# Performance work log

Measured on AMD Instinct MI355X. Metric: run time of the kernel, lower is better.

## Reference

```python
import jax, jax.numpy as jnp
import numpy as np

NEG_BIG = -9e15
LRELU_SLOPE = 0.2  # alpha

N = 8192
IN_F = 256
OUT_F = 128


def setup_inputs() -> dict:
    key = jax.random.key(0)
    k1, k2, k3, k4 = jax.random.split(key, 4)
    inputs = jax.random.normal(k1, (N, IN_F), dtype=jnp.float32)
    adj = jax.random.randint(k2, (N, N), 0, 2, dtype=jnp.int32)
    # xavier_uniform with gain=1.414
    gain = 1.414
    bW = gain * np.sqrt(6.0 / (IN_F + OUT_F))
    W = jax.random.uniform(k3, (IN_F, OUT_F), minval=-bW, maxval=bW, dtype=jnp.float32)
    ba = gain * np.sqrt(6.0 / (2 * OUT_F + 1))
    a = jax.random.uniform(k4, (2 * OUT_F, 1), minval=-ba, maxval=ba, dtype=jnp.float32)
    return {"inputs": inputs, "adj": adj, "W": W, "a": a}


def reference(inputs, adj, W, a):
    # h: [N, F']
    h = inputs @ W
    # a^T [h_i || h_j] = h_i . a[:F'] + h_j . a[F':]  -- avoids the O(N^2 * 2F') concat
    a1 = a[:OUT_F, 0]   # [F']
    a2 = a[OUT_F:, 0]   # [F']
    s1 = h @ a1         # [N]
    s2 = h @ a2         # [N]
    e = s1[:, None] + s2[None, :]                      # [N, N]
    e = jnp.where(e >= 0, e, LRELU_SLOPE * e)          # LeakyReLU(alpha)
    scores = jnp.where(adj > 0, e, jnp.float32(NEG_BIG))
    attention = jax.nn.softmax(scores, axis=1)         # row softmax; dropout p=0
    h_prime = attention @ h                            # [N, F']
    return jax.nn.elu(h_prime)                         # concat=True -> elu
```

## Files before the change

kernel.cpp:

```cpp
#include <hip/hip_runtime.h>
#include <hip/hip_bf16.h>

#define NN   8192
#define INF_ 256
#define OUTF 128
#define SLOPE 0.2f
#define NJC  4
#define JCHUNK (NN / NJC)
#define NT   (JCHUNK / 128)

typedef float f32x4  __attribute__((ext_vector_type(4)));
typedef float f32x16 __attribute__((ext_vector_type(16)));
typedef short bf16x8 __attribute__((ext_vector_type(8)));
typedef int   i32x4  __attribute__((ext_vector_type(4)));
typedef unsigned short u16;
typedef u16 u16x4 __attribute__((ext_vector_type(4)));

__device__ __forceinline__ u16 f2bf(float f) {
  return __builtin_bit_cast(u16, __float2bfloat16(f));
}


__global__ __launch_bounds__(256) void gat_k0(const int* __restrict__ adj,
                                              unsigned char* __restrict__ bm) {
  const int idx = blockIdx.x * 256 + threadIdx.x;
  const int r  = idx >> 10;
  const int jg = idx & 1023;
  const int* p = adj + (size_t)r * NN + jg * 8;
  i32x4 a0 = *(const i32x4*)p;
  i32x4 a1 = *(const i32x4*)(p + 4);
  unsigned b = 0;
#pragma unroll
  for (int e = 0; e < 4; e++) b |= (a0[e] > 0 ? 1u : 0u) << e;
#pragma unroll
  for (int e = 0; e < 4; e++) b |= (a1[e] > 0 ? 1u : 0u) << (e + 4);
  bm[(size_t)r * 1024 + jg] = (unsigned char)b;
}

__global__ __launch_bounds__(256) void gat_k1(
    const float* __restrict__ X, const float* __restrict__ W,
    const float* __restrict__ a, u16* __restrict__ hbF,
    float* __restrict__ s1, float* __restrict__ s2) {
  __shared__ float xs[32 * INF_];
  const int t = threadIdx.x;
  const int r0 = blockIdx.x * 32;
  {
    const f32x4* src = (const f32x4*)(X + (size_t)r0 * INF_);
    f32x4* dst = (f32x4*)xs;
    for (int i = t; i < 32 * INF_ / 4; i += 256) dst[i] = src[i];
  }
  __syncthreads();
  const int cg = t & 31;
  const int rg = t >> 5;
  float acc[4][4];
#pragma unroll
  for (int i = 0; i < 4; i++)
#pragma unroll
    for (int j = 0; j < 4; j++) acc[i][j] = 0.f;

  for (int k = 0; k < INF_; k += 4) {
    f32x4 xv[4];
#pragma unroll
    for (int i = 0; i < 4; i++) xv[i] = *(const f32x4*)&xs[(rg * 4 + i) * INF_ + k];
#pragma unroll
    for (int kk = 0; kk < 4; kk++) {
      f32x4 wv = *(const f32x4*)&W[(k + kk) * OUTF + cg * 4];
#pragma unroll
      for (int i = 0; i < 4; i++)
#pragma unroll
        for (int j = 0; j < 4; j++) acc[i][j] = fmaf(xv[i][kk], wv[j], acc[i][j]);
    }
  }

  f32x4 a1v = *(const f32x4*)&a[cg * 4];
  f32x4 a2v = *(const f32x4*)&a[OUTF + cg * 4];
  float p1[4], p2[4];
#pragma unroll
  for (int i = 0; i < 4; i++) {
    p1[i] = acc[i][0] * a1v[0] + acc[i][1] * a1v[1] + acc[i][2] * a1v[2] + acc[i][3] * a1v[3];
    p2[i] = acc[i][0] * a2v[0] + acc[i][1] * a2v[1] + acc[i][2] * a2v[2] + acc[i][3] * a2v[3];
  }
#pragma unroll
  for (int m = 1; m < 32; m <<= 1) {
#pragma unroll
    for (int i = 0; i < 4; i++) {
      p1[i] += __shfl_xor(p1[i], m);
      p2[i] += __shfl_xor(p2[i], m);
    }
  }
  if (cg == 0) {
#pragma unroll
    for (int i = 0; i < 4; i++) {
      s1[r0 + rg * 4 + i] = p1[i];
      s2[r0 + rg * 4 + i] = p2[i];
    }
  }

  const int R0 = r0 + rg * 4;
  const int jg = (R0 & 2047) >> 3;
  const int tt = jg & 15;
  const int pr = jg >> 4;
  const int wq = pr >> 1;
  const int gg = pr & 1;
  const int e0 = R0 & 7;
  const int n  = ((R0 >> 11) * 16 + tt) * 8 + wq;
#pragma unroll
  for (int j = 0; j < 4; j++) {
    const int C = cg * 4 + j;
    u16x4 pk;
#pragma unroll
    for (int i = 0; i < 4; i++) pk[i] = f2bf(acc[i][j]);
    size_t flat = ((size_t)(n * 4 + (C >> 5)) * 64 + (C & 31) + 32 * gg) * 8 + e0;
    *(u16x4*)(hbF + flat) = pk;
  }
}

__global__ __launch_bounds__(256) void gat_k2(const float* __restrict__ s2,
                                              float* __restrict__ s2m) {
  __shared__ float sm[4];
  const int t = threadIdx.x;
  float m = -1e30f;
  for (int i = t; i < NN; i += 256) m = fmaxf(m, s2[i]);
#pragma unroll
  for (int k = 1; k < 64; k <<= 1) m = fmaxf(m, __shfl_xor(m, k));
  if ((t & 63) == 0) sm[t >> 6] = m;
  __syncthreads();
  if (t == 0) *s2m = fmaxf(fmaxf(sm[0], sm[1]), fmaxf(sm[2], sm[3]));
}

__device__ __forceinline__ void st16(float* dst, const f32x16& A, int g) {
#pragma unroll
  for (int r = 0; r < 16; r++) {
    const int dr = (r & 3) + 8 * (r >> 2) + 4 * g;
    dst[dr * 128] = A[r];
  }
}
__device__ __forceinline__ void ad16(float* dst, const f32x16& A, int g) {
#pragma unroll
  for (int r = 0; r < 16; r++) {
    const int dr = (r & 3) + 8 * (r >> 2) + 4 * g;
    dst[dr * 128] += A[r];
  }
}

__global__ __launch_bounds__(512, 2) void gat_k3(
    const unsigned char* __restrict__ bm, const u16* __restrict__ hbF,
    const float* __restrict__ s1g, const float* __restrict__ s2g,
    const float* __restrict__ s2maxp, float* __restrict__ part,
    float* __restrict__ dpart) {
  __shared__ float lred[8192];
  __shared__ float dred[256];
  const int t = threadIdx.x;
  const int w = t >> 6;
  const int l = t & 63;
  const int rb = blockIdx.x & 255;
  const int jc = blockIdx.x >> 8;
  const int r0 = rb * 32;
  const int row = l & 31;
  const int g = l >> 5;

  const float s1r = s1g[r0 + row];
  const float s2m = *s2maxp;
  float Mi = s1r + s2m;
  Mi = fmaxf(Mi, SLOPE * Mi);
  const float ar = s1r - Mi;
  const float br = SLOPE * s1r - Mi;

  const int pr = 2 * w + g;
  const i32x4 bmv = *(const i32x4*)(bm + (size_t)(r0 + row) * 1024 +
                                    jc * 256 + pr * 16);

  f32x16 acc0 = 0.f, acc1 = 0.f, acc2 = 0.f, acc3 = 0.f;

  const float* sp = s2g + jc * JCHUNK + pr * 128;
  const bf16x8* bp = (const bf16x8*)hbF + ((size_t)(jc * 128 + w) * 4) * 64 + l;

  float dsum = 0.f;
#pragma unroll
  for (int q4 = 0; q4 < 4; q4++) {
    const unsigned word = (unsigned)bmv[q4];
#pragma unroll
    for (int ti = 0; ti < 4; ti++) {
      const int tt = q4 * 4 + ti;
      const unsigned b = (word >> (ti * 8)) & 0xffu;
      const bf16x8* bq = bp + (size_t)tt * 2048;
      bf16x8 b0 = bq[0], b1 = bq[64], b2 = bq[128], b3 = bq[192];
      f32x4 s0  = *(const f32x4*)(sp + 8 * tt);
      f32x4 s1v = *(const f32x4*)(sp + 8 * tt + 4);

      bf16x8 af;
#pragma unroll
      for (int e = 0; e < 8; e++) {
        const float sv = (e < 4) ? s0[e] : s1v[e - 4];
        const float y = fmaxf(ar + sv, fmaf(SLOPE, sv, br));
        float p = __expf(y);
        p = ((b >> e) & 1u) ? p : 0.f;
        dsum += p;
        af[e] = (short)f2bf(p);
      }
      acc0 = __builtin_amdgcn_mfma_f32_32x32x16_bf16(af, b0, acc0, 0, 0, 0);
      acc1 = __builtin_amdgcn_mfma_f32_32x32x16_bf16(af, b1, acc1, 0, 0, 0);
      acc2 = __builtin_amdgcn_mfma_f32_32x32x16_bf16(af, b2, acc2, 0, 0, 0);
      acc3 = __builtin_amdgcn_mfma_f32_32x32x16_bf16(af, b3, acc3, 0, 0, 0);
    }
  }

  dsum += __shfl_xor(dsum, 32);
  if (l < 32) dred[w * 32 + l] = dsum;

  const int colw = l & 31;
  if (w < 2) {
    st16(&lred[w * 4096 + 0 * 32 + colw], acc0, g);
    st16(&lred[w * 4096 + 1 * 32 + colw], acc1, g);
    st16(&lred[w * 4096 + 2 * 32 + colw], acc2, g);
    st16(&lred[w * 4096 + 3 * 32 + colw], acc3, g);
  }
  __syncthreads();
  if (t < 32) {
    float d = 0.f;
#pragma unroll
    for (int w8 = 0; w8 < 8; w8++) d += dred[w8 * 32 + t];
    dpart[jc * NN + r0 + t] = d;
  }
  if (w == 2 || w == 3) {
    ad16(&lred[(w - 2) * 4096 + 0 * 32 + colw], acc0, g);
    ad16(&lred[(w - 2) * 4096 + 1 * 32 + colw], acc1, g);
    ad16(&lred[(w - 2) * 4096 + 2 * 32 + colw], acc2, g);
    ad16(&lred[(w - 2) * 4096 + 3 * 32 + colw], acc3, g);
  }
  __syncthreads();
  if (w == 4 || w == 5) {
    ad16(&lred[(w - 4) * 4096 + 0 * 32 + colw], acc0, g);
    ad16(&lred[(w - 4) * 4096 + 1 * 32 + colw], acc1, g);
    ad16(&lred[(w - 4) * 4096 + 2 * 32 + colw], acc2, g);
    ad16(&lred[(w - 4) * 4096 + 3 * 32 + colw], acc3, g);
  }
  __syncthreads();
  if (w == 6 || w == 7) {
    ad16(&lred[(w - 6) * 4096 + 0 * 32 + colw], acc0, g);
    ad16(&lred[(w - 6) * 4096 + 1 * 32 + colw], acc1, g);
    ad16(&lred[(w - 6) * 4096 + 2 * 32 + colw], acc2, g);
    ad16(&lred[(w - 6) * 4096 + 3 * 32 + colw], acc3, g);
  }
  __syncthreads();

  const int flat = t * 8;
  f32x4 pa = *(f32x4*)&lred[flat];
  f32x4 pb = *(f32x4*)&lred[flat + 4];
  pa += *(f32x4*)&lred[4096 + flat];
  pb += *(f32x4*)&lred[4096 + flat + 4];
  float* pp = part + (size_t)jc * (NN * OUTF) + (size_t)r0 * OUTF + flat;
  *(f32x4*)pp = pa;
  *(f32x4*)(pp + 4) = pb;
}

__global__ __launch_bounds__(256) void gat_k4(
    const float* __restrict__ part, const float* __restrict__ dpart,
    float* __restrict__ out) {
  const int idx = blockIdx.x * 256 + threadIdx.x;
  const int e4 = idx * 4;
  const int i = e4 >> 7;
  f32x4 p = {0.f, 0.f, 0.f, 0.f};
  float d = 0.f;
#pragma unroll
  for (int jc = 0; jc < NJC; jc++) {
    p += *(const f32x4*)&part[(size_t)jc * (NN * OUTF) + e4];
    d += dpart[jc * NN + i];
  }
  d = fmaxf(d, 1e-30f);
  f32x4 r;
#pragma unroll
  for (int k = 0; k < 4; k++) {
    float v = p[k] / d;
    r[k] = (v > 0.f) ? v : expm1f(v);
  }
  *(f32x4*)&out[e4] = r;
}

extern "C" void kernel_launch(void* const* d_in, const int* in_sizes, int n_in,
                              void* d_out, int out_size, void* d_ws, size_t ws_size,
                              hipStream_t stream) {
  (void)in_sizes; (void)n_in; (void)out_size; (void)ws_size;
  const float* X  = (const float*)d_in[0];
  const int*  adj = (const int*)d_in[1];
  const float* W  = (const float*)d_in[2];
  const float* a  = (const float*)d_in[3];
  float* out = (float*)d_out;

  char* ws = (char*)d_ws;
  u16*   hbF   = (u16*)ws;
  float* s1    = (float*)(ws + (2u << 20));
  float* s2    = (float*)(ws + (2u << 20) + (32u << 10));
  float* s2m   = (float*)(ws + (2u << 20) + (64u << 10));
  float* dpart = (float*)(ws + (2u << 20) + (128u << 10));
  unsigned char* bm = (unsigned char*)(ws + (3u << 20));
  float* part  = (float*)(ws + (12u << 20));

  gat_k0<<<NN * 1024 / 256, 256, 0, stream>>>(adj, bm);
  gat_k1<<<NN / 32, 256, 0, stream>>>(X, W, a, hbF, s1, s2);
  gat_k2<<<1, 256, 0, stream>>>(s2, s2m);
  gat_k3<<<256 * NJC, 512, 0, stream>>>(bm, hbF, s1, s2, s2m, part, dpart);
  gat_k4<<<(NN * OUTF / 4) / 256, 256, 0, stream>>>(part, dpart, out);
}
```

Before: 120.0 us.

## Factor per-element exp into precomputed column exponentials and raise occupancy

The main loop computed exp(max(s1-M + s2, 0.2*s1-M + 0.2*s2)) for every (row, col) pair. It now computes max(A*exp(s2), B*exp(0.2*s2)), which removes the per-element transcendental from the hot loop. The column exponentials E1 and E2 are computed once in the s2-max kernel, which now runs with 1024 threads and vector loads. The loop also converts to bf16 with a cheap add-and-byte-permute instead of the library conversion, and raises the minimum-blocks hint to 4. Costs and risks: the hot loop now reads twice as many column values. exp(s2) can overflow or underflow where the fused exponent would not. The stricter occupancy hint may force the 64 accumulator registers to spill.

```diff
diff --git a/kernel.cpp b/kernel.cpp
--- a/kernel.cpp
+++ b/kernel.cpp
@@ -13,6 +13,7 @@
 typedef float f32x16 __attribute__((ext_vector_type(16)));
 typedef short bf16x8 __attribute__((ext_vector_type(8)));
 typedef int   i32x4  __attribute__((ext_vector_type(4)));
+typedef unsigned int u32;
 typedef unsigned short u16;
 typedef u16 u16x4 __attribute__((ext_vector_type(4)));
 
@@ -115,17 +116,35 @@
   }
 }
 
-__global__ __launch_bounds__(256) void gat_k2(const float* __restrict__ s2,
-                                              float* __restrict__ s2m) {
-  __shared__ float sm[4];
+__global__ __launch_bounds__(1024) void gat_k2(const float* __restrict__ s2,
+                                               float* __restrict__ s2m,
+                                               float* __restrict__ E1,
+                                               float* __restrict__ E2) {
+  __shared__ float sm[16];
   const int t = threadIdx.x;
   float m = -1e30f;
-  for (int i = t; i < NN; i += 256) m = fmaxf(m, s2[i]);
+  for (int i = t; i < NN / 4; i += 1024) {
+    f32x4 v = ((const f32x4*)s2)[i];
+    f32x4 e1, e2;
+#pragma unroll
+    for (int k = 0; k < 4; k++) {
+      m = fmaxf(m, v[k]);
+      e1[k] = __expf(v[k]);
+      e2[k] = __expf(SLOPE * v[k]);
+    }
+    ((f32x4*)E1)[i] = e1;
+    ((f32x4*)E2)[i] = e2;
+  }
 #pragma unroll
   for (int k = 1; k < 64; k <<= 1) m = fmaxf(m, __shfl_xor(m, k));
   if ((t & 63) == 0) sm[t >> 6] = m;
   __syncthreads();
-  if (t == 0) *s2m = fmaxf(fmaxf(sm[0], sm[1]), fmaxf(sm[2], sm[3]));
+  if (t == 0) {
+    float mm = sm[0];
+#pragma unroll
+    for (int k = 1; k < 16; k++) mm = fmaxf(mm, sm[k]);
+    *s2m = mm;
+  }
 }
 
 __device__ __forceinline__ void st16(float* dst, const f32x16& A, int g) {
@@ -143,11 +162,11 @@
   }
 }
 
-__global__ __launch_bounds__(512, 2) void gat_k3(
+__global__ __launch_bounds__(512, 4) void gat_k3(
     const unsigned char* __restrict__ bm, const u16* __restrict__ hbF,
-    const float* __restrict__ s1g, const float* __restrict__ s2g,
-    const float* __restrict__ s2maxp, float* __restrict__ part,
-    float* __restrict__ dpart) {
+    const float* __restrict__ s1g, const float* __restrict__ E1,
+    const float* __restrict__ E2, const float* __restrict__ s2maxp,
+    float* __restrict__ part, float* __restrict__ dpart) {
   __shared__ float lred[8192];
   __shared__ float dred[256];
   const int t = threadIdx.x;
@@ -163,8 +182,8 @@
   const float s2m = *s2maxp;
   float Mi = s1r + s2m;
   Mi = fmaxf(Mi, SLOPE * Mi);
-  const float ar = s1r - Mi;
-  const float br = SLOPE * s1r - Mi;
+  const float A = __expf(s1r - Mi);
+  const float B = __expf(SLOPE * s1r - Mi);
 
   const int pr = 2 * w + g;
   const i32x4 bmv = *(const i32x4*)(bm + (size_t)(r0 + row) * 1024 +
@@ -172,38 +191,50 @@
 
   f32x16 acc0 = 0.f, acc1 = 0.f, acc2 = 0.f, acc3 = 0.f;
 
-  const float* sp = s2g + jc * JCHUNK + pr * 128;
+  const float* e1p = E1 + jc * JCHUNK + pr * 128;
+  const float* e2p = E2 + jc * JCHUNK + pr * 128;
   const bf16x8* bp = (const bf16x8*)hbF + ((size_t)(jc * 128 + w) * 4) * 64 + l;
 
-  float dsum = 0.f;
+  float dsA = 0.f, dsB = 0.f;
 #pragma unroll
   for (int q4 = 0; q4 < 4; q4++) {
     const unsigned word = (unsigned)bmv[q4];
 #pragma unroll
     for (int ti = 0; ti < 4; ti++) {
       const int tt = q4 * 4 + ti;
-      const unsigned b = (word >> (ti * 8)) & 0xffu;
+      const unsigned b = word >> (ti * 8);
       const bf16x8* bq = bp + (size_t)tt * 2048;
       bf16x8 b0 = bq[0], b1 = bq[64], b2 = bq[128], b3 = bq[192];
-      f32x4 s0  = *(const f32x4*)(sp + 8 * tt);
-      f32x4 s1v = *(const f32x4*)(sp + 8 * tt + 4);
-
-      bf16x8 af;
-#pragma unroll
-      for (int e = 0; e < 8; e++) {
-        const float sv = (e < 4) ? s0[e] : s1v[e - 4];
-        const float y = fmaxf(ar + sv, fmaf(SLOPE, sv, br));
-        float p = __expf(y);
-        p = ((b >> e) & 1u) ? p : 0.f;
-        dsum += p;
-        af[e] = (short)f2bf(p);
+      f32x4 u0 = *(const f32x4*)(e1p + 8 * tt);
+      f32x4 u1 = *(const f32x4*)(e1p + 8 * tt + 4);
+      f32x4 v0 = *(const f32x4*)(e2p + 8 * tt);
+      f32x4 v1 = *(const f32x4*)(e2p + 8 * tt + 4);
+      const float uu[8] = {u0[0], u0[1], u0[2], u0[3], u1[0], u1[1], u1[2], u1[3]};
+      const float vv[8] = {v0[0], v0[1], v0[2], v0[3], v1[0], v1[1], v1[2], v1[3]};
+
+      u32 aw[4];
+#pragma unroll
+      for (int e = 0; e < 8; e += 2) {
+        float pa = fmaxf(A * uu[e],     B * vv[e]);
+        float pb = fmaxf(A * uu[e + 1], B * vv[e + 1]);
+        pa = (b & (1u << e))       ? pa : 0.f;
+        pb = (b & (1u << (e + 1))) ? pb : 0.f;
+        dsA += pa;
+        dsB += pb;
+        aw[e >> 1] = __builtin_amdgcn_perm(
+            __builtin_bit_cast(u32, pb) + 0x8000u,
+            __builtin_bit_cast(u32, pa) + 0x8000u, 0x07060302u);
       }
+      const bf16x8 af =
+          __builtin_bit_cast(bf16x8, (i32x4){(int)aw[0], (int)aw[1],
+                                             (int)aw[2], (int)aw[3]});
       acc0 = __builtin_amdgcn_mfma_f32_32x32x16_bf16(af, b0, acc0, 0, 0, 0);
       acc1 = __builtin_amdgcn_mfma_f32_32x32x16_bf16(af, b1, acc1, 0, 0, 0);
       acc2 = __builtin_amdgcn_mfma_f32_32x32x16_bf16(af, b2, acc2, 0, 0, 0);
       acc3 = __builtin_amdgcn_mfma_f32_32x32x16_bf16(af, b3, acc3, 0, 0, 0);
     }
   }
+  float dsum = dsA + dsB;
 
   dsum += __shfl_xor(dsum, 32);
   if (l < 32) dred[w * 32 + l] = dsum;
@@ -292,13 +323,15 @@
   float* s1    = (float*)(ws + (2u << 20));
   float* s2    = (float*)(ws + (2u << 20) + (32u << 10));
   float* s2m   = (float*)(ws + (2u << 20) + (64u << 10));
-  float* dpart = (float*)(ws + (2u << 20) + (128u << 10));
+  float* E1    = (float*)(ws + (2u << 20) + (128u << 10));
+  float* E2    = (float*)(ws + (2u << 20) + (160u << 10));
+  float* dpart = (float*)(ws + (2u << 20) + (192u << 10));
   unsigned char* bm = (unsigned char*)(ws + (3u << 20));
   float* part  = (float*)(ws + (12u << 20));
 
   gat_k0<<<NN * 1024 / 256, 256, 0, stream>>>(adj, bm);
   gat_k1<<<NN / 32, 256, 0, stream>>>(X, W, a, hbF, s1, s2);
-  gat_k2<<<1, 256, 0, stream>>>(s2, s2m);
-  gat_k3<<<256 * NJC, 512, 0, stream>>>(bm, hbF, s1, s2, s2m, part, dpart);
+  gat_k2<<<1, 1024, 0, stream>>>(s2, s2m, E1, E2);
+  gat_k3<<<256 * NJC, 512, 0, stream>>>(bm, hbF, s1, E1, E2, s2m, part, dpart);
   gat_k4<<<(NN * OUTF / 4) / 256, 256, 0, stream>>>(part, dpart, out);
 }
```

New measurement: 114.1 us. 1.05x faster.
